# Kernel optimization log

Hardware: AMD Instinct MI355X
Metric: run time of the kernel (lower is better)

## Reference

```python
import jax, jax.numpy as jnp
import numpy as np

SIZE = 1024      # codebook entries
CODE_DIM = 256   # embedding dim


def setup_inputs() -> dict:
    key = jax.random.key(0)
    k_z, k_w = jax.random.split(key)
    z = jax.random.normal(k_z, (8, CODE_DIM, 16, 32, 32), dtype=jnp.float32)
    # init.uniform_(weight, -1/size, 1/size)
    codebook = jax.random.uniform(
        k_w, (SIZE, CODE_DIM), dtype=jnp.float32,
        minval=-1.0 / SIZE, maxval=1.0 / SIZE)
    return {"z": z, "codebook": codebook}


def reference(z, codebook):
    bs, d, t, h, w = z.shape
    # tokens: [N, d] with N = bs*t*h*w (matches permute(0,2,3,4,1).reshape(-1,d))
    zf = jnp.transpose(z, (0, 2, 3, 4, 1)).reshape(-1, d)
    # squared-distance expansion instead of materializing [size, N, d]:
    # ||z - e||^2 = ||z||^2 - 2 z.e + ||e||^2 ; argmin identical to argmin of norm
    d2 = (jnp.sum(zf * zf, axis=1, keepdims=True)
          - 2.0 * (zf @ codebook.T)
          + jnp.sum(codebook * codebook, axis=1))  # [N, size]
    encoding_indices = jnp.argmin(d2, axis=-1).reshape(bs, t, h, w)
    # gather + permute back to [bs, d, t, h, w]
    quantized = jnp.transpose(codebook[encoding_indices], (0, 4, 1, 2, 3))
    st = z + jax.lax.stop_gradient(quantized - z)  # straight-through output
    return (quantized, st, encoding_indices)
```

## Files before the change

### kernel.cpp

```cpp
#include <hip/hip_runtime.h>
#include <stdint.h>


constexpr int Dd  = 256;
constexpr int SPB = 16384;
constexpr int Nn  = 131072;
constexpr int Kk  = 1024;
constexpr int CCAP = 16;
#define WWIN 2.2e-3f

typedef short short8 __attribute__((ext_vector_type(8)));
typedef float v4f    __attribute__((ext_vector_type(4)));

__device__ __forceinline__ unsigned bf16pk(float a, float b){
  unsigned ua = __float_as_uint(a), ub = __float_as_uint(b);
  ua = (ua + 0x7fffu + ((ua >> 16) & 1u)) >> 16;
  ub = (ub + 0x7fffu + ((ub >> 16) & 1u)) & 0xffff0000u;
  return ua | ub;
}
__device__ __forceinline__ short8 frg(uint4 u){
  union { uint4 a; short8 b; } x; x.a = u; return x.b;
}
__device__ __forceinline__ v4f mfma16(short8 a, short8 b, v4f c){
  return __builtin_amdgcn_mfma_f32_16x16x32_bf16(a, b, c, 0, 0, 0);
}
__device__ __forceinline__ void dma16(const void* g, void* l){
  __builtin_amdgcn_global_load_lds((const __attribute__((address_space(1))) void*)g,
                                   (__attribute__((address_space(3))) void*)l, 16, 0, 0);
}

__global__ __launch_bounds__(64) void cnorm_k(const float* __restrict__ cb,
                                              float* __restrict__ cn,
                                              int* __restrict__ heavyCnt){
  const int k = blockIdx.x, l = threadIdx.x;
  if (k == 0 && l == 0) heavyCnt[0] = 0;
  const float* row = cb + (size_t)k * Dd;
  float s = 0.f;
  #pragma unroll
  for (int c = 0; c < Dd; c += 64){ float v = row[c + l]; s += v * v; }
  #pragma unroll
  for (int off = 32; off > 0; off >>= 1) s += __shfl_down(s, off, 64);
  if (l == 0) cn[k] = s;
}

__global__ __launch_bounds__(256) void cconv_k(const float* __restrict__ cb,
                                               uint4* __restrict__ Bg){
  const int cc = blockIdx.x, n = threadIdx.x;
  const float* row = cb + (size_t)(cc * 256 + n) * Dd;
  for (int dc = 0; dc < 8; dc++){
    float v[32];
    const float4* rp = (const float4*)(row + dc * 32);
    #pragma unroll
    for (int q = 0; q < 8; q++){
      float4 f = rp[q]; v[4*q]=f.x; v[4*q+1]=f.y; v[4*q+2]=f.z; v[4*q+3]=f.w;
    }
    unsigned hv[16];
    #pragma unroll
    for (int p = 0; p < 16; p++) hv[p] = bf16pk(v[2*p], v[2*p+1]);
    size_t base = ((size_t)cc * 8 + dc) * 1024;
    #pragma unroll
    for (int kq = 0; kq < 4; kq++)
      Bg[base + (size_t)kq*256 + n] = make_uint4(hv[4*kq],hv[4*kq+1],hv[4*kq+2],hv[4*kq+3]);
  }
}

__global__ __launch_bounds__(512, 4) void vq_sweep_k(const float* __restrict__ z,
                                                     const uint4* __restrict__ Bg,
                                                     const float* __restrict__ cnG,
                                                     int* __restrict__ cntW,
                                                     unsigned short* __restrict__ candW,
                                                     int* __restrict__ abestW,
                                                     int* __restrict__ heavyCnt,
                                                     int* __restrict__ heavyList,
                                                     int* __restrict__ idsW,
                                                     float* __restrict__ out){
  __shared__ uint4 Bs[2][2048];
  __shared__ float cnS[1024];
  __shared__ int hN;
  __shared__ int gBase;
  __shared__ int hT[128];

  const int tid = threadIdx.x, bId = blockIdx.x;
  const int w = tid >> 6, ln = tid & 63;
  const int li = ln & 15, lq = ln >> 4;

  if (tid == 0) hN = 0;

  if (w < 4) dma16((const uint4*)cnG + w*64 + ln, (uint4*)&cnS[w*256]);
  int bOff[4];
  #pragma unroll
  for (int j = 0; j < 4; j++){
    const int f = j*512 + tid;
    bOff[j] = (f >> 8)*1024 + ((f >> 6) & 3)*256 + (f & 63);
  }
  #pragma unroll
  for (int j = 0; j < 4; j++)
    dma16(Bg + bOff[j], &Bs[0][j*512 + w*64]);

  const int tok0 = bId * 128;
  const int b = tok0 >> 14;
  const int s0 = tok0 & 16383;
  const float* zb = z + (size_t)b * Dd * SPB + s0;
  short8 aF[8];
  const int tl = w*16 + li;
  #pragma unroll
  for (int kk = 0; kk < 8; kk++){
    float v[8];
    #pragma unroll
    for (int j = 0; j < 8; j++)
      v[j] = zb[(size_t)(kk*32 + lq*8 + j) * SPB + tl];
    union { unsigned u[4]; short8 s8; } x;
    #pragma unroll
    for (int p = 0; p < 4; p++) x.u[p] = bf16pk(v[2*p], v[2*p+1]);
    aF[kk] = x.s8;
  }

  unsigned bestR[4], thrU[4]; int cntR[4];
  #pragma unroll
  for (int i = 0; i < 4; i++){ bestR[i] = 0xFFFFFFFFu; thrU[i] = 0u; cntR[i] = 0; }

  for (int c = 0; c < 16; c++){
    if (c < 15){
      const int cn1 = c + 1;
      const int srcB = (cn1 >> 2)*8192 + (cn1 & 3)*64;
      uint4* dstB = &Bs[cn1 & 1][0];
      #pragma unroll
      for (int j = 0; j < 4; j++)
        dma16(Bg + srcB + bOff[j], dstB + j*512 + w*64);
      asm volatile("s_waitcnt vmcnt(4)" ::: "memory");
    } else {
      asm volatile("s_waitcnt vmcnt(0)" ::: "memory");
    }
    __builtin_amdgcn_s_barrier();
    asm volatile("" ::: "memory");

    v4f acc[4];
    const v4f vz = {0.f, 0.f, 0.f, 0.f};
    #pragma unroll
    for (int ni = 0; ni < 4; ni++) acc[ni] = vz;

    const uint4* Bbase = &Bs[c & 1][lq*64 + li];
    __builtin_amdgcn_s_setprio(1);
    #pragma unroll
    for (int kk = 0; kk < 8; kk++){
      short8 b0 = frg(Bbase[kk*256 +  0]);
      short8 b1 = frg(Bbase[kk*256 + 16]);
      short8 b2 = frg(Bbase[kk*256 + 32]);
      short8 b3 = frg(Bbase[kk*256 + 48]);
      acc[0] = mfma16(aF[kk], b0, acc[0]);
      acc[1] = mfma16(aF[kk], b1, acc[1]);
      acc[2] = mfma16(aF[kk], b2, acc[2]);
      acc[3] = mfma16(aF[kk], b3, acc[3]);
    }
    __builtin_amdgcn_s_setprio(0);

    float cnv[4];
    #pragma unroll
    for (int ni = 0; ni < 4; ni++) cnv[ni] = cnS[c*64 + ni*16 + li];

    const int codeB = c*64 + li;
    #pragma unroll
    for (int r = 0; r < 4; r++){
      unsigned pv[4];
      unsigned pm = 0xFFFFFFFFu;
      #pragma unroll
      for (int ni = 0; ni < 4; ni++){
        float s = fmaf(acc[ni][r], -2.0f, cnv[ni]);
        unsigned u = __float_as_uint(s);
        u ^= (unsigned)((int)u >> 31) | 0x80000000u;
        unsigned p = (u & 0xFFFFFC00u) | (unsigned)(codeB + ni*16);
        pv[ni] = p;
        pm = (pm < p) ? pm : p;
      }
      unsigned pmw = pm;
      #pragma unroll
      for (int off = 1; off < 16; off <<= 1){
        unsigned o = (unsigned)__shfl_xor((int)pmw, off, 16);
        pmw = (pmw < o) ? pmw : o;
      }
      if (pmw <= bestR[r]){
        bestR[r] = pmw;
        unsigned bp = pmw & 0xFFFFFC00u;
        unsigned fb = (bp & 0x80000000u) ? (bp ^ 0x80000000u) : ~bp;
        float thrf = __uint_as_float(fb) + WWIN;
        unsigned tu = __float_as_uint(thrf);
        tu ^= (unsigned)((int)tu >> 31) | 0x80000000u;
        thrU[r] = tu | 1023u;
      }
      if (__any(pm <= thrU[r])){
        const int tok = tok0 + w*16 + lq*4 + r;
        int base = cntR[r];
        #pragma unroll
        for (int ni = 0; ni < 4; ni++){
          const unsigned p = pv[ni];
          const bool pass = (p <= thrU[r]);
          unsigned long long bal = __ballot(pass);
          const unsigned bq = (unsigned)(bal >> (lq*16)) & 0xFFFFu;
          if (pass){
            int pos = base + __popc(bq & ((1u << li) - 1u));
            if (pos < CCAP)
              candW[(size_t)tok*CCAP + pos] = (unsigned short)(p & 1023u);
          }
          base += __popc(bq);
        }
        cntR[r] = base;
      }
    }
    __builtin_amdgcn_s_barrier();
    asm volatile("" ::: "memory");
  }

  if (li == 0){
    #pragma unroll
    for (int r = 0; r < 4; r++){
      const int tok = tok0 + w*16 + lq*4 + r;
      if (cntR[r] == 1){
        const int code = (int)(bestR[r] & 1023u);
        idsW[tok] = code;
        out[(size_t)2 * Nn * Dd + tok] = (float)code;
      } else {
        int p = atomicAdd(&hN, 1);
        hT[p] = tok;
        cntW[tok] = cntR[r];
        abestW[tok] = (int)(bestR[r] & 1023u);
      }
    }
  }
  __syncthreads();
  if (tid == 0) gBase = hN ? atomicAdd(heavyCnt, hN) : 0;
  __syncthreads();
  if (tid < hN) heavyList[gBase + tid] = hT[tid];
}

__global__ __launch_bounds__(256) void vq_rescore_k(const float* __restrict__ z,
                                                    const float* __restrict__ cb,
                                                    const float* __restrict__ cnG,
                                                    const int* __restrict__ cntW,
                                                    const unsigned short* __restrict__ candW,
                                                    const int* __restrict__ abestW,
                                                    const int* __restrict__ heavyCnt,
                                                    const int* __restrict__ heavyList,
                                                    int* __restrict__ idsW,
                                                    float* __restrict__ out){
  const int hc = heavyCnt[0];
  for (int i = blockIdx.x * 256 + threadIdx.x; i < hc; i += gridDim.x * 256){
    const int tok = heavyList[i];
    const int b = tok >> 14, s = tok & 16383;
    const float* zr = z + (size_t)b * Dd * SPB + s;

    int n = cntW[tok];
    const bool ovf = (n > CCAP);
    if (ovf) n = CCAP;
    unsigned short cds[CCAP];
    *(uint4*)&cds[0] = *(const uint4*)&candW[(size_t)tok * CCAP];
    *(uint4*)&cds[8] = *(const uint4*)&candW[(size_t)tok * CCAP + 8];

    float bv = 3.4e38f; int bi = 0x7fffffff;
    float znl = 0.f;
    const int ngroups = (n + 3) >> 2;
    const int total = ovf ? ngroups + 1 : ngroups;

    for (int g = 0; g < total; g++){
      int idxs[4];
      #pragma unroll
      for (int ss = 0; ss < 4; ss++){
        int slot = g*4 + ss; if (slot >= n) slot = n - 1;
        idxs[ss] = (g < ngroups) ? (int)cds[slot] : abestW[tok];
      }
      const float* cr0 = cb + (size_t)idxs[0] * Dd;
      const float* cr1 = cb + (size_t)idxs[1] * Dd;
      const float* cr2 = cb + (size_t)idxs[2] * Dd;
      const float* cr3 = cb + (size_t)idxs[3] * Dd;
      float a0=0.f, a1=0.f, a2=0.f, a3=0.f, za=0.f;
      for (int d = 0; d < Dd; d += 8){
        float zv[8];
        #pragma unroll
        for (int j = 0; j < 8; j++) zv[j] = zr[(size_t)(d + j) * SPB];
        float4 c0a = *(const float4*)(cr0 + d), c0b = *(const float4*)(cr0 + d + 4);
        float4 c1a = *(const float4*)(cr1 + d), c1b = *(const float4*)(cr1 + d + 4);
        float4 c2a = *(const float4*)(cr2 + d), c2b = *(const float4*)(cr2 + d + 4);
        float4 c3a = *(const float4*)(cr3 + d), c3b = *(const float4*)(cr3 + d + 4);
        float cv0[8] = {c0a.x,c0a.y,c0a.z,c0a.w,c0b.x,c0b.y,c0b.z,c0b.w};
        float cv1[8] = {c1a.x,c1a.y,c1a.z,c1a.w,c1b.x,c1b.y,c1b.z,c1b.w};
        float cv2[8] = {c2a.x,c2a.y,c2a.z,c2a.w,c2b.x,c2b.y,c2b.z,c2b.w};
        float cv3[8] = {c3a.x,c3a.y,c3a.z,c3a.w,c3b.x,c3b.y,c3b.z,c3b.w};
        #pragma unroll
        for (int j = 0; j < 8; j++){
          if (g == 0) za = fmaf(zv[j], zv[j], za);
          a0 = fmaf(zv[j], cv0[j], a0);
          a1 = fmaf(zv[j], cv1[j], a1);
          a2 = fmaf(zv[j], cv2[j], a2);
          a3 = fmaf(zv[j], cv3[j], a3);
        }
      }
      if (g == 0) znl = za;
      float av[4] = {a0, a1, a2, a3};
      const int lim = (g < ngroups) ? n : 1;
      #pragma unroll
      for (int ss = 0; ss < 4; ss++){
        if (g*4 + ss < lim || (g >= ngroups && ss == 0)){
          float t  = znl - 2.0f * av[ss];
          float d2 = t + cnG[idxs[ss]];
          if (d2 < bv || (d2 == bv && idxs[ss] < bi)){ bv = d2; bi = idxs[ss]; }
        }
      }
    }
    idsW[tok] = bi;
    out[(size_t)2 * Nn * Dd + tok] = (float)bi;
  }
}

__global__ __launch_bounds__(256) void vq_gather_k(const float* __restrict__ cb,
                                                   const int* __restrict__ idsW,
                                                   float* __restrict__ out){
  __shared__ float tile[64][129];
  __shared__ int lid[64];
  const int tid = threadIdx.x, blk = blockIdx.x;
  const int b = blk >> 8, s0 = (blk & 255) * 64;
  if (tid < 64) lid[tid] = idsW[b * SPB + s0 + tid];
  __syncthreads();

  const int r2 = tid >> 7, c = tid & 127;
  const int s = tid & 63, cq = tid >> 6;
  float* qb  = out + (size_t)b * Dd * SPB + s0 + s;
  float* stb = qb + (size_t)Nn * Dd;

  for (int ch = 0; ch < 2; ch++){
    #pragma unroll 4
    for (int t0 = 0; t0 < 64; t0 += 2){
      const int row = t0 + r2;
      tile[row][c] = cb[(size_t)lid[row] * Dd + ch*128 + c];
    }
    __syncthreads();
    #pragma unroll 8
    for (int i = 0; i < 32; i++){
      const int cc2 = i*4 + cq;
      const float v = tile[s][cc2];
      const size_t off = (size_t)(ch*128 + cc2) * SPB;
      qb[off]  = v;
      stb[off] = v;
    }
    __syncthreads();
  }
}

#define MICRO_STEP(WITH_ZN)                                                    \
    {                                                                          \
        float4 a0 = *(const float4*)&As[d][ty * 8];                            \
        float4 a1 = *(const float4*)&As[d][ty * 8 + 4];                        \
        float4 b0 = *(const float4*)&Bs[d][tx * 8];                            \
        float4 b1 = *(const float4*)&Bs[d][tx * 8 + 4];                        \
        float a[8] = {a0.x, a0.y, a0.z, a0.w, a1.x, a1.y, a1.z, a1.w};         \
        float bb[8] = {b0.x, b0.y, b0.z, b0.w, b1.x, b1.y, b1.z, b1.w};        \
        _Pragma("unroll")                                                      \
        for (int i = 0; i < 8; i++) {                                          \
            _Pragma("unroll")                                                  \
            for (int j = 0; j < 8; j++) acc[i][j] += a[i] * bb[j];             \
            if (WITH_ZN) zn[i] += a[i] * a[i];                                 \
        }                                                                      \
    }

__global__ __launch_bounds__(256) void vq_k(const float* __restrict__ z,
                                            const float* __restrict__ cb,
                                            const float* __restrict__ cn,
                                            float* __restrict__ out){
  __shared__ float As[16][128];
  __shared__ float Bs[16][132];
  __shared__ int   idsf[128];
  const int tid = threadIdx.x;
  const int tx = tid & 15, ty = tid >> 4;
  const int blk = blockIdx.x;
  const int b = blk >> 7, sb = (blk & 127) * 128;
  const float* zb = z + (size_t)b * Dd * SPB + sb;
  float bestv[8]; int besti[8]; float zn[8];
  #pragma unroll
  for (int i = 0; i < 8; i++){ bestv[i] = 3.4e38f; besti[i] = 0; zn[i] = 0.f; }
  const int am = tid & 127, ad = tid >> 7;
  const int bd = tid & 15,  bk = tid >> 4;
  for (int cc = 0; cc < 8; cc++){
    float acc[8][8];
    #pragma unroll
    for (int i = 0; i < 8; i++)
      #pragma unroll
      for (int j = 0; j < 8; j++) acc[i][j] = 0.f;
    for (int dc = 0; dc < 16; dc++){
      #pragma unroll
      for (int r = 0; r < 8; r++){
        const int d = ad + r * 2;
        As[d][am] = zb[(size_t)(dc*16 + d) * SPB + am];
      }
      #pragma unroll
      for (int r = 0; r < 8; r++){
        const int k = bk + r * 16;
        Bs[bd][k] = cb[(size_t)(cc*128 + k) * Dd + dc*16 + bd];
      }
      __syncthreads();
      if (cc == 0){
        #pragma unroll
        for (int d = 0; d < 16; d++) MICRO_STEP(1)
      } else {
        #pragma unroll
        for (int d = 0; d < 16; d++) MICRO_STEP(0)
      }
      __syncthreads();
    }
    const float* cnp = cn + cc*128 + tx*8;
    float4 c0 = *(const float4*)cnp;
    float4 c1 = *(const float4*)(cnp + 4);
    float cv[8] = {c0.x, c0.y, c0.z, c0.w, c1.x, c1.y, c1.z, c1.w};
    #pragma unroll
    for (int i = 0; i < 8; i++){
      #pragma unroll
      for (int j = 0; j < 8; j++){
        float t  = zn[i] - 2.0f * acc[i][j];
        float d2 = t + cv[j];
        int   ix = cc*128 + tx*8 + j;
        if (d2 < bestv[i]){ bestv[i] = d2; besti[i] = ix; }
      }
    }
  }
  #pragma unroll
  for (int i = 0; i < 8; i++){
    float v = bestv[i]; int ix = besti[i];
    #pragma unroll
    for (int off = 8; off > 0; off >>= 1){
      float ov = __shfl_down(v, off, 16);
      int   oi = __shfl_down(ix, off, 16);
      if (ov < v || (ov == v && oi < ix)){ v = ov; ix = oi; }
    }
    if (tx == 0) idsf[ty*8 + i] = ix;
  }
  __syncthreads();
  if (tid < 128) out[(size_t)2*Nn*Dd + (size_t)blk*128 + tid] = (float)idsf[tid];
  const int m = tid & 127, cg = tid >> 7;
  const int myidx = idsf[m];
  const float* crow = cb + (size_t)myidx * Dd + cg*128;
  float* q  = out + (size_t)b * Dd * SPB + (size_t)cg * 128 * SPB + sb + m;
  float* st = q + (size_t)Nn * Dd;
  #pragma unroll 8
  for (int r = 0; r < 128; r++){
    const float v = crow[r];
    q[(size_t)r * SPB]  = v;
    st[(size_t)r * SPB] = v;
  }
}

extern "C" void kernel_launch(void* const* d_in, const int* in_sizes, int n_in,
                              void* d_out, int out_size, void* d_ws, size_t ws_size,
                              hipStream_t stream){
  const float* z  = (const float*)d_in[0];
  const float* cb = (const float*)d_in[1];
  float* out = (float*)d_out;

  const size_t BG_B  = (size_t)4 * 8 * 1024 * 16;
  const size_t CN_B  = (size_t)Kk * 4;
  const size_t CNT_B = (size_t)Nn * 4;
  const size_t CAN_B = (size_t)Nn * CCAP * 2;
  const size_t ABW_B = (size_t)Nn * 4;
  const size_t IDS_B = (size_t)Nn * 4;
  const size_t HC_B  = 256;
  const size_t HL_B  = (size_t)Nn * 4;
  const size_t NEED = BG_B + CN_B + CNT_B + CAN_B + ABW_B + IDS_B + HC_B + HL_B;

  if (ws_size >= NEED){
    uint8_t* ws = (uint8_t*)d_ws;
    size_t o = 0;
    uint4* Bg   = (uint4*)(ws + o);          o += BG_B;
    float* cnG  = (float*)(ws + o);          o += CN_B;
    int*   cntW = (int*)(ws + o);            o += CNT_B;
    unsigned short* candW = (unsigned short*)(ws + o); o += CAN_B;
    int*   abW  = (int*)(ws + o);            o += ABW_B;
    int*   idsW = (int*)(ws + o);            o += IDS_B;
    int*   hCnt = (int*)(ws + o);            o += HC_B;
    int*   hLst = (int*)(ws + o);            o += HL_B;

    cnorm_k<<<Kk, 64, 0, stream>>>(cb, cnG, hCnt);
    cconv_k<<<4, 256, 0, stream>>>(cb, Bg);
    vq_sweep_k<<<Nn/128, 512, 0, stream>>>(z, Bg, cnG, cntW, candW, abW,
                                           hCnt, hLst, idsW, out);
    vq_rescore_k<<<Nn/256, 256, 0, stream>>>(z, cb, cnG, cntW, candW, abW,
                                             hCnt, hLst, idsW, out);
    vq_gather_k<<<Nn/64, 256, 0, stream>>>(cb, idsW, out);
  } else {
    float* cn = (float*)d_ws;
    cnorm_k<<<Kk, 64, 0, stream>>>(cb, cn, (int*)(cn + Kk));
    vq_k<<<Nn/128, 256, 0, stream>>>(z, cb, cn, out);
  }
}
```

Before: 687.2 us.

## Rescore ambiguous tokens per sweep block with LDS-staged z tiles

Replaces the global atomic heavy-token list with a per-block count and region written by the sweep kernel. The rescore kernel now runs one block per 128-token region, stages z in shared memory in coalesced chunks, and has each heavy token's thread accumulate all candidate dot products in registers. The aim is to remove strided uncoalesced z reads and the global atomic. In exchange, blocks with few heavy tokens still load the whole z tile, and many of the launched blocks exit early.

```diff
diff --git a/kernel.cpp b/kernel.cpp
--- a/kernel.cpp
+++ b/kernel.cpp
@@ -30,10 +30,8 @@
 }
 
 __global__ __launch_bounds__(64) void cnorm_k(const float* __restrict__ cb,
-                                              float* __restrict__ cn,
-                                              int* __restrict__ heavyCnt){
+                                              float* __restrict__ cn){
   const int k = blockIdx.x, l = threadIdx.x;
-  if (k == 0 && l == 0) heavyCnt[0] = 0;
   const float* row = cb + (size_t)k * Dd;
   float s = 0.f;
   #pragma unroll
@@ -70,14 +68,13 @@
                                                      int* __restrict__ cntW,
                                                      unsigned short* __restrict__ candW,
                                                      int* __restrict__ abestW,
-                                                     int* __restrict__ heavyCnt,
-                                                     int* __restrict__ heavyList,
+                                                     int* __restrict__ hCntB,
+                                                     int* __restrict__ heavyRegion,
                                                      int* __restrict__ idsW,
                                                      float* __restrict__ out){
   __shared__ uint4 Bs[2][2048];
   __shared__ float cnS[1024];
   __shared__ int hN;
-  __shared__ int gBase;
   __shared__ int hT[128];
 
   const int tid = threadIdx.x, bId = blockIdx.x;
@@ -227,9 +224,8 @@
     }
   }
   __syncthreads();
-  if (tid == 0) gBase = hN ? atomicAdd(heavyCnt, hN) : 0;
-  __syncthreads();
-  if (tid < hN) heavyList[gBase + tid] = hT[tid];
+  if (tid == 0) hCntB[bId] = hN;
+  if (tid < hN) heavyRegion[bId*128 + tid] = hT[tid];
 }
 
 __global__ __launch_bounds__(256) void vq_rescore_k(const float* __restrict__ z,
@@ -238,72 +234,103 @@
                                                     const int* __restrict__ cntW,
                                                     const unsigned short* __restrict__ candW,
                                                     const int* __restrict__ abestW,
-                                                    const int* __restrict__ heavyCnt,
-                                                    const int* __restrict__ heavyList,
+                                                    const int* __restrict__ hCntB,
+                                                    const int* __restrict__ heavyRegion,
                                                     int* __restrict__ idsW,
                                                     float* __restrict__ out){
-  const int hc = heavyCnt[0];
-  for (int i = blockIdx.x * 256 + threadIdx.x; i < hc; i += gridDim.x * 256){
-    const int tok = heavyList[i];
-    const int b = tok >> 14, s = tok & 16383;
-    const float* zr = z + (size_t)b * Dd * SPB + s;
-
-    int n = cntW[tok];
-    const bool ovf = (n > CCAP);
+  __shared__ float zS[64][128];
+  const int tid = threadIdx.x, reg = blockIdx.x;
+  const int h = hCntB[reg];
+  if (h == 0) return;
+
+  const int tok0 = reg * 128;
+  const int b = tok0 >> 14, sb = tok0 & 16383;
+  const float* zb = z + (size_t)b * Dd * SPB + sb;
+
+  const bool act = tid < h;
+  int tok = 0, tl = 0, n = 0, abest = 0;
+  bool ovf = false;
+  unsigned short cds[CCAP];
+  if (act){
+    tok = heavyRegion[reg*128 + tid];
+    tl = tok & 127;
+    n = cntW[tok];
+    ovf = (n > CCAP);
     if (ovf) n = CCAP;
-    unsigned short cds[CCAP];
     *(uint4*)&cds[0] = *(const uint4*)&candW[(size_t)tok * CCAP];
     *(uint4*)&cds[8] = *(const uint4*)&candW[(size_t)tok * CCAP + 8];
-
+    abest = abestW[tok];
+  }
+  const int eIdx = act ? (ovf ? abest : (int)cds[0]) : 0;
+
+  float accs[CCAP];
+  #pragma unroll
+  for (int i = 0; i < CCAP; i++) accs[i] = 0.f;
+  float accE = 0.f, za = 0.f;
+
+  for (int ch = 0; ch < 4; ch++){
+    if (ch) __syncthreads();
+    #pragma unroll
+    for (int rr = 0; rr < 8; rr++){
+      const int f4 = rr*256 + tid;
+      const int row = f4 >> 5, c4 = f4 & 31;
+      const float4 v = *(const float4*)(zb + (size_t)(ch*64 + row) * SPB + c4*4);
+      *(float4*)&zS[row][c4*4] = v;
+    }
+    __syncthreads();
+    if (act){
+      #pragma unroll 8
+      for (int d = 0; d < 64; d++){
+        const float v = zS[d][tl];
+        za = fmaf(v, v, za);
+      }
+      #pragma unroll
+      for (int ci = 0; ci < CCAP; ci++){
+        if (ci < n){
+          const float* cr = cb + (size_t)cds[ci] * Dd + ch*64;
+          float a = accs[ci];
+          #pragma unroll
+          for (int d = 0; d < 64; d += 4){
+            const float4 cv = *(const float4*)(cr + d);
+            a = fmaf(zS[d+0][tl], cv.x, a);
+            a = fmaf(zS[d+1][tl], cv.y, a);
+            a = fmaf(zS[d+2][tl], cv.z, a);
+            a = fmaf(zS[d+3][tl], cv.w, a);
+          }
+          accs[ci] = a;
+        }
+      }
+      if (ovf){
+        const float* cr = cb + (size_t)eIdx * Dd + ch*64;
+        float a = accE;
+        #pragma unroll
+        for (int d = 0; d < 64; d += 4){
+          const float4 cv = *(const float4*)(cr + d);
+          a = fmaf(zS[d+0][tl], cv.x, a);
+          a = fmaf(zS[d+1][tl], cv.y, a);
+          a = fmaf(zS[d+2][tl], cv.z, a);
+          a = fmaf(zS[d+3][tl], cv.w, a);
+        }
+        accE = a;
+      }
+    }
+  }
+
+  if (act){
     float bv = 3.4e38f; int bi = 0x7fffffff;
-    float znl = 0.f;
-    const int ngroups = (n + 3) >> 2;
-    const int total = ovf ? ngroups + 1 : ngroups;
-
-    for (int g = 0; g < total; g++){
-      int idxs[4];
-      #pragma unroll
-      for (int ss = 0; ss < 4; ss++){
-        int slot = g*4 + ss; if (slot >= n) slot = n - 1;
-        idxs[ss] = (g < ngroups) ? (int)cds[slot] : abestW[tok];
-      }
-      const float* cr0 = cb + (size_t)idxs[0] * Dd;
-      const float* cr1 = cb + (size_t)idxs[1] * Dd;
-      const float* cr2 = cb + (size_t)idxs[2] * Dd;
-      const float* cr3 = cb + (size_t)idxs[3] * Dd;
-      float a0=0.f, a1=0.f, a2=0.f, a3=0.f, za=0.f;
-      for (int d = 0; d < Dd; d += 8){
-        float zv[8];
-        #pragma unroll
-        for (int j = 0; j < 8; j++) zv[j] = zr[(size_t)(d + j) * SPB];
-        float4 c0a = *(const float4*)(cr0 + d), c0b = *(const float4*)(cr0 + d + 4);
-        float4 c1a = *(const float4*)(cr1 + d), c1b = *(const float4*)(cr1 + d + 4);
-        float4 c2a = *(const float4*)(cr2 + d), c2b = *(const float4*)(cr2 + d + 4);
-        float4 c3a = *(const float4*)(cr3 + d), c3b = *(const float4*)(cr3 + d + 4);
-        float cv0[8] = {c0a.x,c0a.y,c0a.z,c0a.w,c0b.x,c0b.y,c0b.z,c0b.w};
-        float cv1[8] = {c1a.x,c1a.y,c1a.z,c1a.w,c1b.x,c1b.y,c1b.z,c1b.w};
-        float cv2[8] = {c2a.x,c2a.y,c2a.z,c2a.w,c2b.x,c2b.y,c2b.z,c2b.w};
-        float cv3[8] = {c3a.x,c3a.y,c3a.z,c3a.w,c3b.x,c3b.y,c3b.z,c3b.w};
-        #pragma unroll
-        for (int j = 0; j < 8; j++){
-          if (g == 0) za = fmaf(zv[j], zv[j], za);
-          a0 = fmaf(zv[j], cv0[j], a0);
-          a1 = fmaf(zv[j], cv1[j], a1);
-          a2 = fmaf(zv[j], cv2[j], a2);
-          a3 = fmaf(zv[j], cv3[j], a3);
-        }
-      }
-      if (g == 0) znl = za;
-      float av[4] = {a0, a1, a2, a3};
-      const int lim = (g < ngroups) ? n : 1;
-      #pragma unroll
-      for (int ss = 0; ss < 4; ss++){
-        if (g*4 + ss < lim || (g >= ngroups && ss == 0)){
-          float t  = znl - 2.0f * av[ss];
-          float d2 = t + cnG[idxs[ss]];
-          if (d2 < bv || (d2 == bv && idxs[ss] < bi)){ bv = d2; bi = idxs[ss]; }
-        }
-      }
+    #pragma unroll
+    for (int ci = 0; ci < CCAP; ci++){
+      if (ci < n){
+        const int ix = (int)cds[ci];
+        float t  = za - 2.0f * accs[ci];
+        float d2 = t + cnG[ix];
+        if (d2 < bv || (d2 == bv && ix < bi)){ bv = d2; bi = ix; }
+      }
+    }
+    if (ovf){
+      float t  = za - 2.0f * accE;
+      float d2 = t + cnG[eIdx];
+      if (d2 < bv || (d2 == bv && eIdx < bi)){ bv = d2; bi = eIdx; }
     }
     idsW[tok] = bi;
     out[(size_t)2 * Nn * Dd + tok] = (float)bi;
@@ -458,9 +485,9 @@
   const size_t CAN_B = (size_t)Nn * CCAP * 2;
   const size_t ABW_B = (size_t)Nn * 4;
   const size_t IDS_B = (size_t)Nn * 4;
-  const size_t HC_B  = 256;
-  const size_t HL_B  = (size_t)Nn * 4;
-  const size_t NEED = BG_B + CN_B + CNT_B + CAN_B + ABW_B + IDS_B + HC_B + HL_B;
+  const size_t HCB_B = (size_t)(Nn/128) * 4;
+  const size_t HR_B  = (size_t)Nn * 4;
+  const size_t NEED = BG_B + CN_B + CNT_B + CAN_B + ABW_B + IDS_B + HCB_B + HR_B;
 
   if (ws_size >= NEED){
     uint8_t* ws = (uint8_t*)d_ws;
@@ -471,19 +498,19 @@
     unsigned short* candW = (unsigned short*)(ws + o); o += CAN_B;
     int*   abW  = (int*)(ws + o);            o += ABW_B;
     int*   idsW = (int*)(ws + o);            o += IDS_B;
-    int*   hCnt = (int*)(ws + o);            o += HC_B;
-    int*   hLst = (int*)(ws + o);            o += HL_B;
-
-    cnorm_k<<<Kk, 64, 0, stream>>>(cb, cnG, hCnt);
+    int*   hCB  = (int*)(ws + o);            o += HCB_B;
+    int*   hReg = (int*)(ws + o);            o += HR_B;
+
+    cnorm_k<<<Kk, 64, 0, stream>>>(cb, cnG);
     cconv_k<<<4, 256, 0, stream>>>(cb, Bg);
     vq_sweep_k<<<Nn/128, 512, 0, stream>>>(z, Bg, cnG, cntW, candW, abW,
-                                           hCnt, hLst, idsW, out);
-    vq_rescore_k<<<Nn/256, 256, 0, stream>>>(z, cb, cnG, cntW, candW, abW,
-                                             hCnt, hLst, idsW, out);
+                                           hCB, hReg, idsW, out);
+    vq_rescore_k<<<Nn/128, 256, 0, stream>>>(z, cb, cnG, cntW, candW, abW,
+                                             hCB, hReg, idsW, out);
     vq_gather_k<<<Nn/64, 256, 0, stream>>>(cb, idsW, out);
   } else {
     float* cn = (float*)d_ws;
-    cnorm_k<<<Kk, 64, 0, stream>>>(cb, cn, (int*)(cn + Kk));
+    cnorm_k<<<Kk, 64, 0, stream>>>(cb, cn);
     vq_k<<<Nn/128, 256, 0, stream>>>(z, cb, cn, out);
   }
 }
```

After: 606.7 us. -11.7%, faster.
